# Optimization experiments

Hardware: AMD Instinct MI355X
Metric: run time of the kernel (lower is better)

## Reference

```python
import jax, jax.numpy as jnp
import numpy as np

N_NODES = 50000
N_EDGES = 500000
IN_DIM = 128
OUT_DIM = 128
T_DIM = 1
NUM_ROUTING = 3
NUM_PERSP = 4
BETA = -1.0
EPSILON = 1e-12
ACOSH_MIN = 1.0 + 1e-6
CLIP_VAL = 10000.0
MAX_TANH_VAL = 10.0


def _inner(x, y):
    # pseudo-Riemannian inner product, time dims negated; keepdims
    return (-jnp.sum(x[..., :T_DIM] * y[..., :T_DIM], axis=-1, keepdims=True)
            + jnp.sum(x[..., T_DIM:] * y[..., T_DIM:], axis=-1, keepdims=True))


def _log_map(x, ref):
    x = jnp.clip(x, -CLIP_VAL, CLIP_VAL)
    inner = _inner(x, ref)
    ref_sq = _inner(ref, ref)
    x_sq = _inner(x, x)
    denom = jnp.sqrt(jnp.clip(jnp.abs(ref_sq * x_sq), EPSILON, None))
    cos_dist = jnp.clip(-inner / denom, ACOSH_MIN, None)
    dist = jnp.arccosh(cos_dist)
    sin_dist = jnp.clip(jnp.sqrt(cos_dist ** 2 - 1.0), EPSILON, None)
    coef = dist / sin_dist
    return coef * (x + (inner / ref_sq) * ref)


def _exp_map(v, ref):
    v_norm = jnp.clip(jnp.sqrt(jnp.abs(_inner(v, v)) + EPSILON), None, MAX_TANH_VAL)
    return jnp.cosh(v_norm) * ref + (jnp.sinh(v_norm) / v_norm) * v


def _squash(s):
    norm_sq = jnp.sum(s ** 2, axis=-1, keepdims=True)
    scale = norm_sq / (1.0 + norm_sq)
    return scale * (s / jnp.sqrt(norm_sq + 1e-9))


def setup_inputs() -> dict:
    key = jax.random.key(0)
    ks = jax.random.split(key, 7)
    x = jax.random.normal(ks[0], (N_NODES, IN_DIM), dtype=jnp.float32)
    edge_index = jax.random.randint(ks[1], (2, N_EDGES), 0, N_NODES, dtype=jnp.int32)
    lim1 = 1.0 / np.sqrt(IN_DIM)
    W_per = jax.random.uniform(ks[2], (IN_DIM, OUT_DIM * NUM_PERSP), jnp.float32, -lim1, lim1)
    b_per = jax.random.uniform(ks[3], (OUT_DIM * NUM_PERSP,), jnp.float32, -lim1, lim1)
    W_gate = jax.random.uniform(ks[4], (IN_DIM, NUM_PERSP), jnp.float32, -lim1, lim1)
    b_gate = jax.random.uniform(ks[5], (NUM_PERSP,), jnp.float32, -lim1, lim1)
    bias = jnp.zeros((1, OUT_DIM), dtype=jnp.float32)
    return {"x": x, "edge_index": edge_index, "W_per": W_per, "b_per": b_per,
            "W_gate": W_gate, "b_gate": b_gate, "bias": bias}


def reference(x, edge_index, W_per, b_per, W_gate, b_gate, bias):
    N = x.shape[0]
    row, col = edge_index[0], edge_index[1]
    # pole: beta=-1 -> sqrt(|beta|) in time slot 0
    ref = jnp.zeros((1, x.shape[1]), x.dtype).at[0, 0].set(np.sqrt(abs(BETA)))
    x_tangent = _log_map(x, ref)              # dropout is identity in eval mode
    xc = x_tangent[row]                        # [E, in_dim]
    u_k = (xc @ W_per + b_per).reshape(-1, NUM_PERSP, OUT_DIM)
    gate = jax.nn.softmax(xc @ W_gate + b_gate, axis=-1)[..., None]
    u_hat = jnp.sum(u_k * gate, axis=1)        # [E, out_dim]
    u_b = u_hat + bias
    b_ij = jnp.zeros(row.shape[0], x.dtype)
    s_j = jnp.zeros((N, OUT_DIM), x.dtype)
    for r in range(NUM_ROUTING):
        m = jax.ops.segment_max(b_ij, col, num_segments=N)
        e = jnp.exp(b_ij - m[col])
        z = jax.ops.segment_sum(e, col, num_segments=N)
        c_ij = e / z[col]                      # scatter_softmax over col
        s_j = jax.ops.segment_sum(c_ij[:, None] * u_b, col, num_segments=N)
        s_j = _squash(s_j)
        if r < NUM_ROUTING - 1:
            b_ij = b_ij + jnp.sum(s_j[col] * u_hat, axis=-1)
    return _exp_map(s_j, ref)
```

## Files before the change

kernel.cpp:

```cpp
#include <hip/hip_runtime.h>
#include <hip/hip_fp16.h>
#include <hip/hip_bf16.h>

typedef short bf16x8 __attribute__((ext_vector_type(8)));
typedef float f32x4 __attribute__((ext_vector_type(4)));
typedef _Float16 f16x2 __attribute__((ext_vector_type(2)));

#define LGKM_FENCE() asm volatile("s_waitcnt lgkmcnt(0)" ::: "memory")
#define CAP 32

static __device__ __forceinline__ f16x2 as_f16x2(uint v) {
  union { uint u; f16x2 h; } c; c.u = v; return c.h;
}

static __device__ __forceinline__ float dot2acc(uint a, uint b, float c) {
#if __has_builtin(__builtin_amdgcn_fdot2)
  return __builtin_amdgcn_fdot2(as_f16x2(a), as_f16x2(b), c, false);
#else
  float2 af = __half22float2(*(const __half2*)&a);
  float2 bf = __half22float2(*(const __half2*)&b);
  return fmaf(af.x, bf.x, fmaf(af.y, bf.y, c));
#endif
}

__global__ __launch_bounds__(256) void k_tangent_gate(
    const float* __restrict__ x, const float* __restrict__ Wg,
    const float* __restrict__ bg, __hip_bfloat16* __restrict__ xtb,
    float* __restrict__ gate, const float* __restrict__ Wp,
    __hip_bfloat16* __restrict__ Wt, int N) {
  int tb = (N + 3) >> 2;
  if ((int)blockIdx.x >= tb) {
    int idx = (blockIdx.x - tb) * 256 + threadIdx.x;
    if (idx < 512 * 128) {
      int n = idx >> 7, k = idx & 127;
      Wt[idx] = __float2bfloat16(Wp[(size_t)k * 512 + n]);
    }
    return;
  }
  int wid = (blockIdx.x * blockDim.x + threadIdx.x) >> 6;
  int lane = threadIdx.x & 63;
  if (wid >= N) return;

  const float* xr = x + (size_t)wid * 128;
  float2 xv = *(const float2*)(xr + lane * 2);
  xv.x = fminf(fmaxf(xv.x, -10000.f), 10000.f);
  xv.y = fminf(fmaxf(xv.y, -10000.f), 10000.f);

  float p = xv.x * xv.x + xv.y * xv.y;
  if (lane == 0) p -= 2.f * xv.x * xv.x;
  #pragma unroll
  for (int s = 32; s; s >>= 1) p += __shfl_xor(p, s);
  float x0 = __shfl(xv.x, 0);

  float denom = sqrtf(fmaxf(fabsf(p), 1e-12f));
  float cosd = fmaxf(x0 / denom, 1.0f + 1e-6f);
  float t = cosd - 1.0f;
  float coef = (t < 1e-3f)
      ? 1.0f - t * (1.f / 3.f) + t * t * (2.f / 15.f)
      : acoshf(cosd) * rsqrtf(t * (2.f + t));

  float2 o;
  o.x = coef * ((lane == 0) ? 2.0f * xv.x : xv.x);
  o.y = coef * xv.y;
  __hip_bfloat162 hb = __float22bfloat162_rn(make_float2(o.x, o.y));
  *(__hip_bfloat162*)(xtb + (size_t)wid * 128 + lane * 2) = hb;

  const float4 w0 = *(const float4*)(Wg + (size_t)(lane * 2) * 4);
  const float4 w1 = *(const float4*)(Wg + (size_t)(lane * 2 + 1) * 4);
  float g0 = o.x * w0.x + o.y * w1.x;
  float g1 = o.x * w0.y + o.y * w1.y;
  float g2 = o.x * w0.z + o.y * w1.z;
  float g3 = o.x * w0.w + o.y * w1.w;
  #pragma unroll
  for (int s = 32; s; s >>= 1) {
    g0 += __shfl_xor(g0, s); g1 += __shfl_xor(g1, s);
    g2 += __shfl_xor(g2, s); g3 += __shfl_xor(g3, s);
  }
  g0 += bg[0]; g1 += bg[1]; g2 += bg[2]; g3 += bg[3];
  float m = fmaxf(fmaxf(g0, g1), fmaxf(g2, g3));
  float e0 = expf(g0 - m), e1 = expf(g1 - m), e2 = expf(g2 - m), e3 = expf(g3 - m);
  float z = e0 + e1 + e2 + e3;
  if (lane == 0)
    *(float4*)(gate + (size_t)wid * 4) = make_float4(e0 / z, e1 / z, e2 / z, e3 / z);
}

#define TPB 4
__global__ __launch_bounds__(256, 2) void k_uhat_mfma(
    const short* __restrict__ xtb, const float* __restrict__ gate,
    const short* __restrict__ Wt, const float* __restrict__ bp,
    __half* __restrict__ uh, const int* __restrict__ row,
    const int* __restrict__ col, int* __restrict__ cnt,
    int* __restrict__ slots, int* __restrict__ ovf_cnt,
    int2* __restrict__ ovf, int N, int ntiles, int E) {
  int ub = (ntiles + TPB - 1) / TPB;
  if ((int)blockIdx.x >= ub) {
    int e0 = ((blockIdx.x - ub) * 256 + threadIdx.x) * 2;
    #pragma unroll
    for (int k = 0; k < 2; ++k) {
      int e = e0 + k;
      if (e < E) {
        int c = col[e];
        int p = atomicAdd(&cnt[c], 1);
        if (p < CAP) slots[(size_t)c * CAP + p] = row[e];
        else { int q = atomicAdd(ovf_cnt, 1); ovf[q] = make_int2(c, row[e]); }
      }
    }
    return;
  }

  int lane = threadIdx.x & 63;
  int wv = threadIdx.x >> 6;
  int ri = lane & 15, kg = lane >> 4;
  int c_lo = wv * 32;

  bf16x8 bfr[4][2][4];
  float bpv[4][2];
  #pragma unroll
  for (int p = 0; p < 4; ++p)
    #pragma unroll
    for (int n2 = 0; n2 < 2; ++n2) {
      int bcol = p * 128 + c_lo + n2 * 16 + ri;
      #pragma unroll
      for (int ks = 0; ks < 4; ++ks)
        bfr[p][n2][ks] = *(const bf16x8*)(Wt + (((size_t)bcol) << 7) + ks * 32 + kg * 8);
      bpv[p][n2] = bp[bcol];
    }

  int t0 = blockIdx.x * TPB;

  bf16x8 af[TPB][4];
  #pragma unroll
  for (int tt = 0; tt < TPB; ++tt) {
    int t = t0 + tt;
    int r0 = t * 16 + ri;
    int c0 = (t < ntiles) ? ((r0 < N) ? r0 : (N - 1)) : 0;
    #pragma unroll
    for (int ks = 0; ks < 4; ++ks)
      af[tt][ks] = *(const bf16x8*)(xtb + (((size_t)c0) << 7) + ks * 32 + kg * 8);
  }

  #pragma unroll
  for (int tt = 0; tt < TPB; ++tt) {
    int t = t0 + tt;
    if (t < ntiles) {
      int m0 = t * 16;
      int rb = m0 + kg * 4;
      float gg[4][4];
      #pragma unroll
      for (int q = 0; q < 4; ++q) {
        int rm = rb + q;
        bool ok = rm < N;
        float4 gv = *(const float4*)(gate + (size_t)(ok ? rm : 0) * 4);
        gg[q][0] = ok ? gv.x : 0.f;
        gg[q][1] = ok ? gv.y : 0.f;
        gg[q][2] = ok ? gv.z : 0.f;
        gg[q][3] = ok ? gv.w : 0.f;
      }

      float fin[2][4];
      #pragma unroll
      for (int n2 = 0; n2 < 2; ++n2)
        #pragma unroll
        for (int q = 0; q < 4; ++q) fin[n2][q] = 0.f;

      #pragma unroll
      for (int p = 0; p < 4; ++p)
        #pragma unroll
        for (int n2 = 0; n2 < 2; ++n2) {
          f32x4 acc = {0.f, 0.f, 0.f, 0.f};
          #pragma unroll
          for (int ks = 0; ks < 4; ++ks)
            acc = __builtin_amdgcn_mfma_f32_16x16x32_bf16(af[tt][ks], bfr[p][n2][ks], acc, 0, 0, 0);
          #pragma unroll
          for (int q = 0; q < 4; ++q)
            fin[n2][q] += gg[q][p] * (acc[q] + bpv[p][n2]);
        }

      #pragma unroll
      for (int n2 = 0; n2 < 2; ++n2) {
        int cn = c_lo + n2 * 16 + ri;
        #pragma unroll
        for (int q = 0; q < 4; ++q) {
          int rm = rb + q;
          if (rm < N) uh[(size_t)rm * 128 + cn] = __float2half_rn(fin[n2][q]);
        }
      }
    }
  }
}

__global__ __launch_bounds__(64, 4) void k_route(
    const __half* __restrict__ uh, const float* __restrict__ bias,
    const int* __restrict__ cnt, const int* __restrict__ slots,
    const int* __restrict__ ovf_cnt, const int2* __restrict__ ovf,
    int* __restrict__ fbc, int* __restrict__ claim,
    int* __restrict__ fb_rows, float* __restrict__ fb_b,
    float* __restrict__ out, int N) {
  __shared__ __align__(16) uint ssw[64];
  int lane = threadIdx.x;
  int j = blockIdx.x;
  int deg = cnt[j];
  int d0 = lane * 2;

  if (deg == 0) {
    *(float2*)(out + (size_t)j * 128 + d0) =
        make_float2((lane == 0) ? 1.f : 0.f, 0.f);
    return;
  }

  float2 bia = *(const float2*)(bias + d0);
  float s0 = 0.f, s1 = 0.f;
  const uint* uhw = (const uint*)uh;

  if (deg <= 16) {
    int myrow = (lane < deg) ? slots[(size_t)j * CAP + lane] : 0;

    int e = lane >> 2, q = lane & 3;
    int er = __shfl(myrow, (e < deg) ? e : 0);
    const uint4* up = (const uint4*)(uhw + (((size_t)(uint)er) << 6) + q * 16);
    uint4 ud4[4];
    #pragma unroll
    for (int w4 = 0; w4 < 4; ++w4) ud4[w4] = up[w4];

    uint g[16];
    #pragma unroll
    for (int c = 0; c < 16; c += 8) {
      if (c < deg) {
        #pragma unroll
        for (int k = 0; k < 8; ++k) {
          int i = c + k;
          int rr = __builtin_amdgcn_readlane(myrow, i);
          uint v = uhw[(((size_t)(uint)rr) << 6) + lane];
          g[i] = (i < deg) ? v : 0u;
        }
      }
    }

    float2 uf[16];
    float a0 = 0.f, a1 = 0.f;
    #pragma unroll
    for (int c = 0; c < 16; c += 8) {
      if (c < deg) {
        #pragma unroll
        for (int k = 0; k < 8; ++k) {
          int i = c + k;
          uf[i] = __half22float2(*(const __half2*)&g[i]);
          a0 += uf[i].x; a1 += uf[i].y;
        }
      }
    }

    float invd = 1.f / (float)deg;
    s0 = a0 * invd + bia.x;
    s1 = a1 * invd + bia.y;
    {
      float ns = s0 * s0 + s1 * s1;
      #pragma unroll
      for (int s = 32; s; s >>= 1) ns += __shfl_xor(ns, s);
      float scale = (ns / (1.f + ns)) * rsqrtf(ns + 1e-9f);
      s0 *= scale; s1 *= scale;
    }

    const uint* ssw_q = &ssw[q * 16];
    bool act = (e < deg);
    float b = 0.f;

    #pragma unroll
    for (int r = 0; r < 2; ++r) {
      __half2 sh2 = __floats2half2_rn(s0, s1);
      ssw[lane] = *(const uint*)&sh2;
      LGKM_FENCE();

      float acc0 = 0.f, acc1 = 0.f;
      #pragma unroll
      for (int w4 = 0; w4 < 4; ++w4) {
        uint4 sw = *(const uint4*)&ssw_q[w4 * 4];
        acc0 = dot2acc(ud4[w4].x, sw.x, acc0);
        acc1 = dot2acc(ud4[w4].y, sw.y, acc1);
        acc0 = dot2acc(ud4[w4].z, sw.z, acc0);
        acc1 = dot2acc(ud4[w4].w, sw.w, acc1);
      }
      float acc = acc0 + acc1;
      acc += __shfl_xor(acc, 1);
      acc += __shfl_xor(acc, 2);
      b += acc;
      float eb = act ? __expf(b) : 0.f;

      float z0 = 0.f, z1 = 0.f, wa0 = 0.f, wa1 = 0.f, wb0 = 0.f, wb1 = 0.f;
      #pragma unroll
      for (int c = 0; c < 16; c += 8) {
        if (c < deg) {
          #pragma unroll
          for (int k = 0; k < 8; ++k) {
            int i = c + k;
            float ev = __uint_as_float(
                __builtin_amdgcn_readlane(__float_as_uint(eb), 4 * i));
            if (k & 1) { z1 += ev; wa1 = fmaf(ev, uf[i].x, wa1); wb1 = fmaf(ev, uf[i].y, wb1); }
            else       { z0 += ev; wa0 = fmaf(ev, uf[i].x, wa0); wb0 = fmaf(ev, uf[i].y, wb0); }
          }
        }
      }
      float z = z0 + z1;
      float invz = 1.f / z;
      s0 = (wa0 + wa1) * invz + bia.x;
      s1 = (wb0 + wb1) * invz + bia.y;
      float ns = s0 * s0 + s1 * s1;
      #pragma unroll
      for (int s = 32; s; s >>= 1) ns += __shfl_xor(ns, s);
      float scale = (ns / (1.f + ns)) * rsqrtf(ns + 1e-9f);
      s0 *= scale; s1 *= scale;
    }
  } else if (deg <= CAP) {
    int myrow = (lane < deg) ? slots[(size_t)j * CAP + lane] : 0;

    int e = lane >> 1, h = lane & 1;
    int er = __shfl(myrow, (e < deg) ? e : 0);
    const uint4* up = (const uint4*)(uhw + (((size_t)(uint)er) << 6) + h * 32);
    uint4 ud[8];
    #pragma unroll
    for (int k4 = 0; k4 < 8; ++k4) ud[k4] = up[k4];

    uint g[CAP];
    #pragma unroll
    for (int c = 0; c < CAP; c += 8) {
      if (c < deg) {
        #pragma unroll
        for (int k = 0; k < 8; ++k) {
          int i = c + k;
          int rr = __builtin_amdgcn_readlane(myrow, i);
          uint v = uhw[(((size_t)(uint)rr) << 6) + lane];
          g[i] = (i < deg) ? v : 0u;
        }
      }
    }

    float a0 = 0.f, a1 = 0.f;
    #pragma unroll
    for (int c = 0; c < CAP; c += 8) {
      if (c < deg) {
        #pragma unroll
        for (int k = 0; k < 8; ++k) {
          int i = c + k;
          float2 uf = __half22float2(*(const __half2*)&g[i]);
          a0 += uf.x; a1 += uf.y;
        }
      }
    }

    float invd = 1.f / (float)deg;
    s0 = a0 * invd + bia.x;
    s1 = a1 * invd + bia.y;
    {
      float ns = s0 * s0 + s1 * s1;
      #pragma unroll
      for (int s = 32; s; s >>= 1) ns += __shfl_xor(ns, s);
      float scale = (ns / (1.f + ns)) * rsqrtf(ns + 1e-9f);
      s0 *= scale; s1 *= scale;
    }

    const uint* ssw_h = &ssw[h * 32];
    bool act = (e < deg);
    float b = 0.f;

    #pragma unroll
    for (int r = 0; r < 2; ++r) {
      __half2 sh2 = __floats2half2_rn(s0, s1);
      ssw[lane] = *(const uint*)&sh2;
      LGKM_FENCE();

      float acc0 = 0.f, acc1 = 0.f;
      #pragma unroll
      for (int k4 = 0; k4 < 8; ++k4) {
        uint4 sw = *(const uint4*)&ssw_h[k4 * 4];
        acc0 = dot2acc(ud[k4].x, sw.x, acc0);
        acc1 = dot2acc(ud[k4].y, sw.y, acc1);
        acc0 = dot2acc(ud[k4].z, sw.z, acc0);
        acc1 = dot2acc(ud[k4].w, sw.w, acc1);
      }
      float acc = acc0 + acc1;
      acc += __shfl_xor(acc, 1);
      b += acc;
      float eb = act ? __expf(b) : 0.f;

      float z0 = 0.f, z1 = 0.f, wa0 = 0.f, wa1 = 0.f, wb0 = 0.f, wb1 = 0.f;
      #pragma unroll
      for (int c = 0; c < CAP; c += 8) {
        if (c < deg) {
          #pragma unroll
          for (int k = 0; k < 8; ++k) {
            int i = c + k;
            float ev = __uint_as_float(
                __builtin_amdgcn_readlane(__float_as_uint(eb), 2 * i));
            float2 uf = __half22float2(*(const __half2*)&g[i]);
            if (k & 1) { z1 += ev; wa1 = fmaf(ev, uf.x, wa1); wb1 = fmaf(ev, uf.y, wb1); }
            else       { z0 += ev; wa0 = fmaf(ev, uf.x, wa0); wb0 = fmaf(ev, uf.y, wb0); }
          }
        }
      }
      float z = z0 + z1;
      float invz = 1.f / z;
      s0 = (wa0 + wa1) * invz + bia.x;
      s1 = (wb0 + wb1) * invz + bia.y;
      float ns = s0 * s0 + s1 * s1;
      #pragma unroll
      for (int s = 32; s; s >>= 1) ns += __shfl_xor(ns, s);
      float scale = (ns / (1.f + ns)) * rsqrtf(ns + 1e-9f);
      s0 *= scale; s1 *= scale;
    }
  } else {
    int base = 0;
    if (lane == 0) base = atomicAdd(claim, deg);
    base = __shfl(base, 0);
    int* mr = fb_rows + base;
    float* b = fb_b + base;
    if (lane < CAP) mr[lane] = slots[(size_t)j * CAP + lane];
    int novf = *ovf_cnt;
    for (int t = lane; t < novf; t += 64) {
      int2 ov = ovf[t];
      if (ov.x == j) {
        int p = atomicAdd(&fbc[j], 1);
        mr[CAP + p] = ov.y;
      }
    }
    asm volatile("s_waitcnt vmcnt(0)" ::: "memory");

    const __half2* uh2 = (const __half2*)uh;
    for (int i = lane; i < deg; i += 64) atomicExch(&b[i], 0.f);
    asm volatile("s_waitcnt vmcnt(0)" ::: "memory");

    for (int r = 0; r < 3; ++r) {
      float mx = -3.4e38f;
      for (int i = lane; i < deg; i += 64)
        mx = fmaxf(mx, atomicAdd(&b[i], 0.f));
      #pragma unroll
      for (int s = 32; s; s >>= 1) mx = fmaxf(mx, __shfl_xor(mx, s));
      float z = 0.f;
      for (int i = lane; i < deg; i += 64) z += expf(atomicAdd(&b[i], 0.f) - mx);
      #pragma unroll
      for (int s = 32; s; s >>= 1) z += __shfl_xor(z, s);
      float invz = 1.f / z;

      s0 = 0.f; s1 = 0.f;
      for (int i = 0; i < deg; ++i) {
        float c = expf(atomicAdd(&b[i], 0.f) - mx) * invz;
        int rr = mr[i];
        float2 uf = __half22float2(uh2[(((size_t)rr) << 6) + lane]);
        s0 = fmaf(c, uf.x, s0);
        s1 = fmaf(c, uf.y, s1);
      }
      s0 += bia.x; s1 += bia.y;

      float ns = s0 * s0 + s1 * s1;
      #pragma unroll
      for (int s = 32; s; s >>= 1) ns += __shfl_xor(ns, s);
      float scale = (ns / (1.f + ns)) * rsqrtf(ns + 1e-9f);
      s0 *= scale; s1 *= scale;

      if (r < 2) {
        for (int i = 0; i < deg; ++i) {
          int rr = mr[i];
          float2 uf = __half22float2(uh2[(((size_t)rr) << 6) + lane]);
          float pp = s0 * uf.x + s1 * uf.y;
          #pragma unroll
          for (int s = 32; s; s >>= 1) pp += __shfl_xor(pp, s);
          if (lane == 0) atomicAdd(&b[i], pp);
        }
        asm volatile("s_waitcnt vmcnt(0)" ::: "memory");
      }
    }
  }

  float pn = s0 * s0 + s1 * s1;
  if (lane == 0) pn -= 2.f * s0 * s0;
  #pragma unroll
  for (int s = 32; s; s >>= 1) pn += __shfl_xor(pn, s);
  float vn = fminf(sqrtf(fabsf(pn) + 1e-12f), 10.f);
  float sh = sinhf(vn) / vn;
  float ov0 = sh * s0 + ((lane == 0) ? coshf(vn) : 0.f);
  float ov1 = sh * s1;
  *(float2*)(out + (size_t)j * 128 + d0) = make_float2(ov0, ov1);
}

extern "C" void kernel_launch(void* const* d_in, const int* in_sizes, int n_in,
                              void* d_out, int out_size, void* d_ws, size_t ws_size,
                              hipStream_t stream) {
  const float* x    = (const float*)d_in[0];
  const int*   ei   = (const int*)d_in[1];
  const float* Wp   = (const float*)d_in[2];
  const float* bp   = (const float*)d_in[3];
  const float* Wg   = (const float*)d_in[4];
  const float* bg   = (const float*)d_in[5];
  const float* bias = (const float*)d_in[6];
  float* out = (float*)d_out;

  int N = in_sizes[0] / 128;
  int E = in_sizes[1] / 2;
  const int* row = ei;
  const int* col = ei + E;

  __hip_bfloat16* xtb = (__hip_bfloat16*)d_ws;
  __half* uhh = (__half*)(xtb + (size_t)N * 128);
  float* gate = (float*)(uhh + (size_t)N * 128);
  __hip_bfloat16* Wt = (__hip_bfloat16*)(gate + (size_t)N * 4);
  int* cnt = (int*)(Wt + 512 * 128);
  int* fbc = cnt + N;
  int* claim = fbc + N;
  int* ovf_cnt = claim + 1;
  int* slots = ovf_cnt + 1;
  int2* ovf = (int2*)(slots + (size_t)N * CAP);
  int* fb_rows = (int*)(ovf + E);
  float* fb_b = (float*)(fb_rows + E);

  int tb = (N + 3) / 4;
  int hb = (E + 511) / 512;
  int ntiles = (N + 15) / 16;
  int ub = (ntiles + TPB - 1) / TPB;
  (void)hipMemsetAsync(cnt, 0, ((size_t)2 * N + 2) * sizeof(int), stream);
  k_tangent_gate<<<tb + 256, 256, 0, stream>>>(x, Wg, bg, xtb, gate, Wp, Wt, N);
  k_uhat_mfma<<<ub + hb, 256, 0, stream>>>(
      (const short*)xtb, gate, (const short*)Wt, bp, uhh,
      row, col, cnt, slots, ovf_cnt, ovf, N, ntiles, E);
  k_route<<<N, 64, 0, stream>>>(
      uhh, bias, cnt, slots, ovf_cnt, ovf, fbc, claim, fb_rows, fb_b, out, N);
}
```

Before: 138.7 us.

## Fold counter zeroing into first kernel and add low-degree routing path

The separate memset of the degree and claim counters is replaced by extra blocks appended to the tangent/gate kernel, which removes one launch from the stream. The routing kernel gains a dedicated path for nodes with degree at most 8. In that path each edge's u_hat row is split across 8 lanes instead of 4, so per-lane register loads and the dot-product reduction depth shrink. This adds code size and another branch. It also depends on the zeroing blocks finishing before the next kernel reads the counters, which stream ordering provides.

```diff
diff --git a/kernel.cpp b/kernel.cpp
--- a/kernel.cpp
+++ b/kernel.cpp
@@ -27,8 +27,14 @@
     const float* __restrict__ x, const float* __restrict__ Wg,
     const float* __restrict__ bg, __hip_bfloat16* __restrict__ xtb,
     float* __restrict__ gate, const float* __restrict__ Wp,
-    __hip_bfloat16* __restrict__ Wt, int N) {
+    __hip_bfloat16* __restrict__ Wt, int* __restrict__ zbase,
+    int nz, int N) {
   int tb = (N + 3) >> 2;
+  if ((int)blockIdx.x >= tb + 256) {
+    int idx = (blockIdx.x - tb - 256) * 256 + threadIdx.x;
+    if (idx < nz) zbase[idx] = 0;
+    return;
+  }
   if ((int)blockIdx.x >= tb) {
     int idx = (blockIdx.x - tb) * 256 + threadIdx.x;
     if (idx < 512 * 128) {
@@ -212,7 +218,87 @@
   float s0 = 0.f, s1 = 0.f;
   const uint* uhw = (const uint*)uh;
 
-  if (deg <= 16) {
+  if (deg <= 8) {
+    int myrow = (lane < deg) ? slots[(size_t)j * CAP + lane] : 0;
+
+    int e = lane >> 3, o = lane & 7;
+    int er = __shfl(myrow, (e < deg) ? e : 0);
+    const uint4* up = (const uint4*)(uhw + (((size_t)(uint)er) << 6) + o * 8);
+    uint4 ud8[2];
+    ud8[0] = up[0]; ud8[1] = up[1];
+
+    uint g[8];
+    #pragma unroll
+    for (int k = 0; k < 8; ++k) {
+      int rr = __builtin_amdgcn_readlane(myrow, k);
+      uint v = uhw[(((size_t)(uint)rr) << 6) + lane];
+      g[k] = (k < deg) ? v : 0u;
+    }
+
+    float2 uf[8];
+    float a0 = 0.f, a1 = 0.f;
+    #pragma unroll
+    for (int k = 0; k < 8; ++k) {
+      uf[k] = __half22float2(*(const __half2*)&g[k]);
+      a0 += uf[k].x; a1 += uf[k].y;
+    }
+
+    float invd = 1.f / (float)deg;
+    s0 = a0 * invd + bia.x;
+    s1 = a1 * invd + bia.y;
+    {
+      float ns = s0 * s0 + s1 * s1;
+      #pragma unroll
+      for (int s = 32; s; s >>= 1) ns += __shfl_xor(ns, s);
+      float scale = (ns / (1.f + ns)) * rsqrtf(ns + 1e-9f);
+      s0 *= scale; s1 *= scale;
+    }
+
+    const uint* ssw_o = &ssw[o * 8];
+    bool act = (e < deg);
+    float b = 0.f;
+
+    #pragma unroll
+    for (int r = 0; r < 2; ++r) {
+      __half2 sh2 = __floats2half2_rn(s0, s1);
+      ssw[lane] = *(const uint*)&sh2;
+      LGKM_FENCE();
+
+      float acc0 = 0.f, acc1 = 0.f;
+      #pragma unroll
+      for (int w4 = 0; w4 < 2; ++w4) {
+        uint4 sw = *(const uint4*)&ssw_o[w4 * 4];
+        acc0 = dot2acc(ud8[w4].x, sw.x, acc0);
+        acc1 = dot2acc(ud8[w4].y, sw.y, acc1);
+        acc0 = dot2acc(ud8[w4].z, sw.z, acc0);
+        acc1 = dot2acc(ud8[w4].w, sw.w, acc1);
+      }
+      float acc = acc0 + acc1;
+      acc += __shfl_xor(acc, 1);
+      acc += __shfl_xor(acc, 2);
+      acc += __shfl_xor(acc, 4);
+      b += acc;
+      float eb = act ? __expf(b) : 0.f;
+
+      float z0 = 0.f, z1 = 0.f, wa0 = 0.f, wa1 = 0.f, wb0 = 0.f, wb1 = 0.f;
+      #pragma unroll
+      for (int k = 0; k < 8; ++k) {
+        float ev = __uint_as_float(
+            __builtin_amdgcn_readlane(__float_as_uint(eb), 8 * k));
+        if (k & 1) { z1 += ev; wa1 = fmaf(ev, uf[k].x, wa1); wb1 = fmaf(ev, uf[k].y, wb1); }
+        else       { z0 += ev; wa0 = fmaf(ev, uf[k].x, wa0); wb0 = fmaf(ev, uf[k].y, wb0); }
+      }
+      float z = z0 + z1;
+      float invz = 1.f / z;
+      s0 = (wa0 + wa1) * invz + bia.x;
+      s1 = (wb0 + wb1) * invz + bia.y;
+      float ns = s0 * s0 + s1 * s1;
+      #pragma unroll
+      for (int s = 32; s; s >>= 1) ns += __shfl_xor(ns, s);
+      float scale = (ns / (1.f + ns)) * rsqrtf(ns + 1e-9f);
+      s0 *= scale; s1 *= scale;
+    }
+  } else if (deg <= 16) {
     int myrow = (lane < deg) ? slots[(size_t)j * CAP + lane] : 0;
 
     int e = lane >> 2, q = lane & 3;
@@ -513,10 +599,12 @@
 
   int tb = (N + 3) / 4;
   int hb = (E + 511) / 512;
+  int nz = 2 * N + 2;
+  int zb = (nz + 255) / 256;
   int ntiles = (N + 15) / 16;
   int ub = (ntiles + TPB - 1) / TPB;
-  (void)hipMemsetAsync(cnt, 0, ((size_t)2 * N + 2) * sizeof(int), stream);
-  k_tangent_gate<<<tb + 256, 256, 0, stream>>>(x, Wg, bg, xtb, gate, Wp, Wt, N);
+  k_tangent_gate<<<tb + 256 + zb, 256, 0, stream>>>(
+      x, Wg, bg, xtb, gate, Wp, Wt, cnt, nz, N);
   k_uhat_mfma<<<ub + hb, 256, 0, stream>>>(
       (const short*)xtb, gate, (const short*)Wt, bp, uhh,
       row, col, cnt, slots, ovf_cnt, ovf, N, ntiles, E);
```

After: 126.9 us (median of 2 runs). 8.5% less time.
